# Optimization experiments

Hardware: AMD Instinct MI355X
Metric: run time of the kernel (lower is better)

## Reference

```python
import jax, jax.numpy as jnp
import numpy as np

NUM_HEADS = 16
LN_EPS = 1e-5


def setup_inputs() -> dict:
    key = jax.random.key(0)
    ks = jax.random.split(key, 5)
    B, S, D = 2, 2048, 1024
    scale = 1.0 / np.sqrt(D)
    return {
        "x": jax.random.normal(ks[0], (B, S, D), dtype=jnp.float32),
        "in_proj_w": jax.random.normal(ks[1], (3 * D, D), dtype=jnp.float32) * scale,
        "in_proj_b": jnp.zeros((3 * D,), dtype=jnp.float32),
        "out_proj_w": jax.random.normal(ks[2], (D, D), dtype=jnp.float32) * scale,
        "out_proj_b": jnp.zeros((D,), dtype=jnp.float32),
        "ln_gamma": jnp.ones((D,), dtype=jnp.float32),
        "ln_beta": jnp.zeros((D,), dtype=jnp.float32),
    }


def reference(x, in_proj_w, in_proj_b, out_proj_w, out_proj_b, ln_gamma, ln_beta):
    # Faithful to nn.MultiheadAttention(batch_first=True, need_weights=True)
    # + residual + LayerNorm. Dropout is identity (eval mode).
    B, S, D = x.shape
    H = NUM_HEADS
    hd = D // H

    qkv = x @ in_proj_w.T + in_proj_b                      # [B,S,3D]
    q, k, v = jnp.split(qkv, 3, axis=-1)
    # [B,S,D] -> [B,H,S,hd]
    q = q.reshape(B, S, H, hd).transpose(0, 2, 1, 3)
    k = k.reshape(B, S, H, hd).transpose(0, 2, 1, 3)
    v = v.reshape(B, S, H, hd).transpose(0, 2, 1, 3)

    scores = jnp.einsum("bhqd,bhkd->bhqk", q, k) / jnp.sqrt(jnp.float32(hd))
    w = jax.nn.softmax(scores, axis=-1)                    # [B,H,S,S]
    ctx = jnp.einsum("bhqk,bhkd->bhqd", w, v)              # [B,H,S,hd]
    ctx = ctx.transpose(0, 2, 1, 3).reshape(B, S, D)
    attn_output = ctx @ out_proj_w.T + out_proj_b          # [B,S,D]

    # residual + LayerNorm (dropout disabled at inference)
    y = x + attn_output
    mu = jnp.mean(y, axis=-1, keepdims=True)
    var = jnp.var(y, axis=-1, keepdims=True)
    out = (y - mu) * jax.lax.rsqrt(var + LN_EPS) * ln_gamma + ln_beta

    # PyTorch default average_attn_weights=True -> mean over heads
    attn_weights = w.mean(axis=1)                          # [B,S,S]
    return (out, attn_weights)
```

## Files before the change

### kernel.cpp

```cpp
#include <hip/hip_runtime.h>
#include <math.h>

constexpr int B = 2, S = 2048, D = 1024, H = 16, HD = 64;
constexpr int T = B * S;
constexpr float EPS = 1e-5f;

typedef float f32x4 __attribute__((ext_vector_type(4)));
typedef __bf16 bf16x8 __attribute__((ext_vector_type(8)));

struct alignas(16) u4 { unsigned x, y, z, w; };
struct alignas(8) u2 { unsigned x, y; };

__device__ __forceinline__ unsigned short f2bf(float f) {
  unsigned u = __float_as_uint(f);
  u += 0x7fffu + ((u >> 16) & 1u);
  return (unsigned short)(u >> 16);
}
__device__ __forceinline__ float bf2f(unsigned short h) {
  return __uint_as_float(((unsigned)h) << 16);
}
__device__ __forceinline__ f32x4 MM(bf16x8 a, bf16x8 b, f32x4 c) {
  return __builtin_amdgcn_mfma_f32_16x16x32_bf16(a, b, c, 0, 0, 0);
}
union U16x8 { u4 q; bf16x8 b; };

__device__ __forceinline__ bf16x8 ld_frag(const unsigned short* lds, int row,
                                          int chunk) {
  U16x8 u;
  u.q = *(const u4*)((const char*)lds + row * 128 +
                     (((chunk) ^ (row & 7)) * 16));
  return u.b;
}

__device__ __forceinline__ void stage64(const unsigned short* __restrict__ src,
                                        size_t off, int rstride,
                                        unsigned short* lds, int tid) {
#pragma unroll
  for (int p = 0; p < 2; ++p) {
    const int idx = tid + p * 256;
    const int r = idx >> 3, c = idx & 7;
    u4 v = *(const u4*)(src + off + (size_t)r * rstride + c * 8);
    *(u4*)((char*)lds + r * 128 + ((c ^ (r & 7)) * 16)) = v;
  }
}

__global__ __launch_bounds__(256) void k_split(const float* __restrict__ src,
                                               unsigned short* __restrict__ hi,
                                               unsigned short* __restrict__ lo,
                                               int n4) {
  const int i = blockIdx.x * 256 + threadIdx.x;
  if (i >= n4) return;
  const float4 v = ((const float4*)src)[i];
  const unsigned short h0 = f2bf(v.x), h1 = f2bf(v.y), h2 = f2bf(v.z),
                       h3 = f2bf(v.w);
  u2 hh, ll;
  hh.x = (unsigned)h0 | ((unsigned)h1 << 16);
  hh.y = (unsigned)h2 | ((unsigned)h3 << 16);
  ll.x = (unsigned)f2bf(v.x - bf2f(h0)) | ((unsigned)f2bf(v.y - bf2f(h1)) << 16);
  ll.y = (unsigned)f2bf(v.z - bf2f(h2)) | ((unsigned)f2bf(v.w - bf2f(h3)) << 16);
  ((u2*)hi)[i] = hh;
  ((u2*)lo)[i] = ll;
}

__global__ __launch_bounds__(256) void k_qkv(
    const unsigned short* __restrict__ xh, const unsigned short* __restrict__ xl,
    const unsigned short* __restrict__ wh, const unsigned short* __restrict__ wl,
    const float* __restrict__ bias,
    unsigned short* __restrict__ Qh, unsigned short* __restrict__ Ql,
    unsigned short* __restrict__ Kh, unsigned short* __restrict__ Kl,
    unsigned short* __restrict__ Vh, unsigned short* __restrict__ Vl) {
  __shared__ unsigned short Ah[4096], Al[4096], Bh[4096], Bl[4096];
  const int tid = threadIdx.x;
  const int w = tid >> 6, lane = tid & 63;
  const int j = lane & 15, g = lane >> 4;
  const int row0 = blockIdx.y * 64;
  const int col0 = blockIdx.x * 64;
  const f32x4 z4 = {0.f, 0.f, 0.f, 0.f};
  f32x4 acc[4] = {z4, z4, z4, z4};

  for (int k0 = 0; k0 < D; k0 += 64) {
    __syncthreads();
    stage64(xh, (size_t)row0 * D + k0, D, Ah, tid);
    stage64(xl, (size_t)row0 * D + k0, D, Al, tid);
    stage64(wh, (size_t)col0 * D + k0, D, Bh, tid);
    stage64(wl, (size_t)col0 * D + k0, D, Bl, tid);
    __syncthreads();
#pragma unroll
    for (int kk = 0; kk < 2; ++kk) {
      const int arow = 16 * w + j;
      const bf16x8 ah = ld_frag(Ah, arow, kk * 4 + g);
      const bf16x8 al = ld_frag(Al, arow, kk * 4 + g);
#pragma unroll
      for (int nf = 0; nf < 4; ++nf) {
        const bf16x8 bh = ld_frag(Bh, 16 * nf + j, kk * 4 + g);
        const bf16x8 bl = ld_frag(Bl, 16 * nf + j, kk * 4 + g);
        acc[nf] = MM(ah, bh, acc[nf]);
        acc[nf] = MM(ah, bl, acc[nf]);
        acc[nf] = MM(al, bh, acc[nf]);
      }
    }
  }

  const int part = col0 >> 10;
  const int h = (col0 & 1023) >> 6;
  if (part < 2) {
    const float qsc = (part == 0) ? 0.125f : 1.0f;
    unsigned short* dh = (part == 0) ? Qh : Kh;
    unsigned short* dl = (part == 0) ? Ql : Kl;
#pragma unroll
    for (int nf = 0; nf < 4; ++nf) {
      const int hd = 16 * nf + j;
      const float bv = bias[col0 + hd];
#pragma unroll
      for (int r = 0; r < 4; ++r) {
        const int tok = row0 + 16 * w + 4 * g + r;
        const int bb = tok >> 11, ss = tok & 2047;
        const float v = (acc[nf][r] + bv) * qsc;
        const unsigned short hh = f2bf(v);
        const size_t o = (((size_t)bb * H + h) * S + ss) * HD + hd;
        dh[o] = hh;
        dl[o] = f2bf(v - bf2f(hh));
      }
    }
  } else {
#pragma unroll
    for (int nf = 0; nf < 4; ++nf) {
      const int hd = 16 * nf + j;
      const float bv = bias[col0 + hd];
      const int tok0 = row0 + 16 * w + 4 * g;
      const int bb = tok0 >> 11, ss = tok0 & 2047;
      const float v0 = acc[nf][0] + bv, v1 = acc[nf][1] + bv;
      const float v2 = acc[nf][2] + bv, v3 = acc[nf][3] + bv;
      const unsigned short h0 = f2bf(v0), h1 = f2bf(v1), h2 = f2bf(v2),
                           h3 = f2bf(v3);
      const size_t o = (((size_t)bb * H + h) * HD + hd) * S + ss;
      u2 ph, pl;
      ph.x = (unsigned)h0 | ((unsigned)h1 << 16);
      ph.y = (unsigned)h2 | ((unsigned)h3 << 16);
      pl.x = (unsigned)f2bf(v0 - bf2f(h0)) | ((unsigned)f2bf(v1 - bf2f(h1)) << 16);
      pl.y = (unsigned)f2bf(v2 - bf2f(h2)) | ((unsigned)f2bf(v3 - bf2f(h3)) << 16);
      *(u2*)(Vh + o) = ph;
      *(u2*)(Vl + o) = pl;
    }
  }
}

__global__ __launch_bounds__(256) void k_ctx(
    const unsigned short* __restrict__ Qh, const unsigned short* __restrict__ Ql,
    const unsigned short* __restrict__ Kh, const unsigned short* __restrict__ Kl,
    const unsigned short* __restrict__ Vh, const unsigned short* __restrict__ Vl,
    unsigned short* __restrict__ ch, unsigned short* __restrict__ cl,
    float* __restrict__ mo, float* __restrict__ lo) {
  __shared__ unsigned short Ksh[4096], Ksl[4096], Vsh[4096], Vsl[4096];
  const int tid = threadIdx.x;
  const int w = tid >> 6, lane = tid & 63;
  const int j = lane & 15, g = lane >> 4;
  const int q0 = blockIdx.x * 64;
  const int h = blockIdx.y, b = blockIdx.z;
  const size_t hb = (size_t)b * H + h;
  const int qrow = q0 + 16 * w + j;

  bf16x8 qfh[2], qfl[2];
#pragma unroll
  for (int kk = 0; kk < 2; ++kk) {
    const size_t o = (hb * S + qrow) * HD + kk * 32 + 8 * g;
    U16x8 u;
    u.q = *(const u4*)(Qh + o);
    qfh[kk] = u.b;
    u.q = *(const u4*)(Ql + o);
    qfl[kk] = u.b;
  }

  const f32x4 z4 = {0.f, 0.f, 0.f, 0.f};
  f32x4 ctxa[4] = {z4, z4, z4, z4};
  float m_run = -INFINITY, l_run = 0.f;

  for (int k0 = 0; k0 < S; k0 += 64) {
    __syncthreads();
    stage64(Kh, (hb * S + k0) * HD, HD, Ksh, tid);
    stage64(Kl, (hb * S + k0) * HD, HD, Ksl, tid);
    stage64(Vh, hb * HD * S + k0, S, Vsh, tid);
    stage64(Vl, hb * HD * S + k0, S, Vsl, tid);
    __syncthreads();

    f32x4 st[4] = {z4, z4, z4, z4};
#pragma unroll
    for (int kk = 0; kk < 2; ++kk) {
#pragma unroll
      for (int kb = 0; kb < 4; ++kb) {
        const bf16x8 ah = ld_frag(Ksh, 16 * kb + j, kk * 4 + g);
        const bf16x8 al = ld_frag(Ksl, 16 * kb + j, kk * 4 + g);
        st[kb] = MM(ah, qfh[kk], st[kb]);
        st[kb] = MM(ah, qfl[kk], st[kb]);
        st[kb] = MM(al, qfh[kk], st[kb]);
      }
    }

    float pm = -INFINITY;
#pragma unroll
    for (int kb = 0; kb < 4; ++kb)
#pragma unroll
      for (int r = 0; r < 4; ++r) pm = fmaxf(pm, st[kb][r]);
    pm = fmaxf(pm, __shfl_xor(pm, 16));
    pm = fmaxf(pm, __shfl_xor(pm, 32));
    const float m_new = fmaxf(m_run, pm);
    const float sc = __expf(m_run - m_new);
    m_run = m_new;
    float p[4][4];
    float ls = 0.f;
#pragma unroll
    for (int kb = 0; kb < 4; ++kb)
#pragma unroll
      for (int r = 0; r < 4; ++r) {
        p[kb][r] = __expf(st[kb][r] - m_new);
        ls += p[kb][r];
      }
    l_run = l_run * sc + ls;
#pragma unroll
    for (int mf = 0; mf < 4; ++mf) ctxa[mf] *= sc;

    unsigned ph[4][2], pl[4][2];
#pragma unroll
    for (int kb = 0; kb < 4; ++kb) {
      const unsigned short a0 = f2bf(p[kb][0]), a1 = f2bf(p[kb][1]);
      const unsigned short a2 = f2bf(p[kb][2]), a3 = f2bf(p[kb][3]);
      ph[kb][0] = (unsigned)a0 | ((unsigned)a1 << 16);
      ph[kb][1] = (unsigned)a2 | ((unsigned)a3 << 16);
      pl[kb][0] = (unsigned)f2bf(p[kb][0] - bf2f(a0)) |
                  ((unsigned)f2bf(p[kb][1] - bf2f(a1)) << 16);
      pl[kb][1] = (unsigned)f2bf(p[kb][2] - bf2f(a2)) |
                  ((unsigned)f2bf(p[kb][3] - bf2f(a3)) << 16);
    }

    const int srcA = ((g & 1) << 5) + j;
    const int srcB = srcA + 16;
    const bool hikb = (g >> 1) != 0;
#pragma unroll
    for (int t = 0; t < 2; ++t) {
      const unsigned w0a = __shfl(ph[2 * t][0], srcA), w0b = __shfl(ph[2 * t + 1][0], srcA);
      const unsigned w1a = __shfl(ph[2 * t][1], srcA), w1b = __shfl(ph[2 * t + 1][1], srcA);
      const unsigned w2a = __shfl(ph[2 * t][0], srcB), w2b = __shfl(ph[2 * t + 1][0], srcB);
      const unsigned w3a = __shfl(ph[2 * t][1], srcB), w3b = __shfl(ph[2 * t + 1][1], srcB);
      U16x8 pbh;
      pbh.q.x = hikb ? w0b : w0a;
      pbh.q.y = hikb ? w1b : w1a;
      pbh.q.z = hikb ? w2b : w2a;
      pbh.q.w = hikb ? w3b : w3a;
      const unsigned v0a = __shfl(pl[2 * t][0], srcA), v0b = __shfl(pl[2 * t + 1][0], srcA);
      const unsigned v1a = __shfl(pl[2 * t][1], srcA), v1b = __shfl(pl[2 * t + 1][1], srcA);
      const unsigned v2a = __shfl(pl[2 * t][0], srcB), v2b = __shfl(pl[2 * t + 1][0], srcB);
      const unsigned v3a = __shfl(pl[2 * t][1], srcB), v3b = __shfl(pl[2 * t + 1][1], srcB);
      U16x8 pbl;
      pbl.q.x = hikb ? v0b : v0a;
      pbl.q.y = hikb ? v1b : v1a;
      pbl.q.z = hikb ? v2b : v2a;
      pbl.q.w = hikb ? v3b : v3a;
#pragma unroll
      for (int mf = 0; mf < 4; ++mf) {
        const bf16x8 vh_ = ld_frag(Vsh, 16 * mf + j, t * 4 + g);
        const bf16x8 vl_ = ld_frag(Vsl, 16 * mf + j, t * 4 + g);
        ctxa[mf] = MM(vh_, pbh.b, ctxa[mf]);
        ctxa[mf] = MM(vh_, pbl.b, ctxa[mf]);
        ctxa[mf] = MM(vl_, pbh.b, ctxa[mf]);
      }
    }
  }

  float lt = l_run;
  lt += __shfl_xor(lt, 16);
  lt += __shfl_xor(lt, 32);
  const float inv = 1.0f / lt;
  const int tokg = b * S + (q0 + 16 * w + j);
#pragma unroll
  for (int mf = 0; mf < 4; ++mf) {
    const int feat = h * HD + 16 * mf + 4 * g;
    const float v0 = ctxa[mf][0] * inv, v1 = ctxa[mf][1] * inv;
    const float v2 = ctxa[mf][2] * inv, v3 = ctxa[mf][3] * inv;
    const unsigned short h0 = f2bf(v0), h1 = f2bf(v1), h2 = f2bf(v2),
                         h3 = f2bf(v3);
    const size_t o = (size_t)tokg * D + feat;
    u2 hh, ll;
    hh.x = (unsigned)h0 | ((unsigned)h1 << 16);
    hh.y = (unsigned)h2 | ((unsigned)h3 << 16);
    ll.x = (unsigned)f2bf(v0 - bf2f(h0)) | ((unsigned)f2bf(v1 - bf2f(h1)) << 16);
    ll.y = (unsigned)f2bf(v2 - bf2f(h2)) | ((unsigned)f2bf(v3 - bf2f(h3)) << 16);
    *(u2*)(ch + o) = hh;
    *(u2*)(cl + o) = ll;
  }
  if (g == 0) {
    mo[hb * S + qrow] = m_run;
    lo[hb * S + qrow] = lt;
  }
}

__global__ __launch_bounds__(256) void k_oproj(
    const unsigned short* __restrict__ ah_, const unsigned short* __restrict__ al_,
    const unsigned short* __restrict__ wh, const unsigned short* __restrict__ wl,
    const float* __restrict__ bias, const float* __restrict__ x,
    float* __restrict__ y) {
  __shared__ unsigned short Ah[4096], Al[4096], Bh[4096], Bl[4096];
  const int tid = threadIdx.x;
  const int w = tid >> 6, lane = tid & 63;
  const int j = lane & 15, g = lane >> 4;
  const int row0 = blockIdx.y * 64;
  const int col0 = blockIdx.x * 64;
  const f32x4 z4 = {0.f, 0.f, 0.f, 0.f};
  f32x4 acc[4] = {z4, z4, z4, z4};

  for (int k0 = 0; k0 < D; k0 += 64) {
    __syncthreads();
    stage64(ah_, (size_t)row0 * D + k0, D, Ah, tid);
    stage64(al_, (size_t)row0 * D + k0, D, Al, tid);
    stage64(wh, (size_t)col0 * D + k0, D, Bh, tid);
    stage64(wl, (size_t)col0 * D + k0, D, Bl, tid);
    __syncthreads();
#pragma unroll
    for (int kk = 0; kk < 2; ++kk) {
      const int arow = 16 * w + j;
      const bf16x8 ah = ld_frag(Ah, arow, kk * 4 + g);
      const bf16x8 al = ld_frag(Al, arow, kk * 4 + g);
#pragma unroll
      for (int nf = 0; nf < 4; ++nf) {
        const bf16x8 bh = ld_frag(Bh, 16 * nf + j, kk * 4 + g);
        const bf16x8 bl = ld_frag(Bl, 16 * nf + j, kk * 4 + g);
        acc[nf] = MM(ah, bh, acc[nf]);
        acc[nf] = MM(ah, bl, acc[nf]);
        acc[nf] = MM(al, bh, acc[nf]);
      }
    }
  }
#pragma unroll
  for (int nf = 0; nf < 4; ++nf) {
    const int col = col0 + 16 * nf + j;
    const float bv = bias[col];
#pragma unroll
    for (int r = 0; r < 4; ++r) {
      const int tok = row0 + 16 * w + 4 * g + r;
      const size_t off = (size_t)tok * D + col;
      y[off] = acc[nf][r] + bv + x[off];
    }
  }
}

__global__ __launch_bounds__(256) void k_wts(
    const unsigned short* __restrict__ Qh, const unsigned short* __restrict__ Ql,
    const unsigned short* __restrict__ Kh, const unsigned short* __restrict__ Kl,
    const float* __restrict__ mi, const float* __restrict__ li,
    float* __restrict__ attn) {
  __shared__ unsigned short Ksh[4096], Ksl[4096];
  const int tid = threadIdx.x;
  const int w = tid >> 6, lane = tid & 63;
  const int j = lane & 15, g = lane >> 4;
  const int k0 = blockIdx.x * 64;
  const int q0 = blockIdx.y * 64;
  const int b = blockIdx.z;
  const f32x4 z4 = {0.f, 0.f, 0.f, 0.f};
  f32x4 wacc[4] = {z4, z4, z4, z4};

  for (int h = 0; h < H; ++h) {
    const size_t hb = (size_t)b * H + h;
    __syncthreads();
    stage64(Kh, (hb * S + k0) * HD, HD, Ksh, tid);
    stage64(Kl, (hb * S + k0) * HD, HD, Ksl, tid);
    __syncthreads();
    bf16x8 qfh[2], qfl[2];
#pragma unroll
    for (int kk = 0; kk < 2; ++kk) {
      const size_t o = (hb * S + q0 + 16 * w + j) * HD + kk * 32 + 8 * g;
      U16x8 u;
      u.q = *(const u4*)(Qh + o);
      qfh[kk] = u.b;
      u.q = *(const u4*)(Ql + o);
      qfl[kk] = u.b;
    }
    f32x4 sacc[4] = {z4, z4, z4, z4};
#pragma unroll
    for (int kk = 0; kk < 2; ++kk) {
#pragma unroll
      for (int nf = 0; nf < 4; ++nf) {
        const bf16x8 kh_ = ld_frag(Ksh, 16 * nf + j, kk * 4 + g);
        const bf16x8 kl_ = ld_frag(Ksl, 16 * nf + j, kk * 4 + g);
        sacc[nf] = MM(qfh[kk], kh_, sacc[nf]);
        sacc[nf] = MM(qfh[kk], kl_, sacc[nf]);
        sacc[nf] = MM(qfl[kk], kh_, sacc[nf]);
      }
    }
    float mr[4], lv[4];
#pragma unroll
    for (int r = 0; r < 4; ++r) {
      const size_t o = hb * S + q0 + 16 * w + 4 * g + r;
      mr[r] = mi[o];
      lv[r] = 1.0f / li[o];
    }
#pragma unroll
    for (int nf = 0; nf < 4; ++nf)
#pragma unroll
      for (int r = 0; r < 4; ++r)
        wacc[nf][r] = fmaf(__expf(sacc[nf][r] - mr[r]), lv[r], wacc[nf][r]);
  }
  const float ih = 1.0f / (float)H;
#pragma unroll
  for (int nf = 0; nf < 4; ++nf)
#pragma unroll
    for (int r = 0; r < 4; ++r) {
      const size_t row = (size_t)b * S + q0 + 16 * w + 4 * g + r;
      attn[row * S + k0 + 16 * nf + j] = wacc[nf][r] * ih;
    }
}

__global__ __launch_bounds__(256) void k_ln(float* __restrict__ y,
                                            const float* __restrict__ gamma,
                                            const float* __restrict__ beta) {
  const int row = blockIdx.x;
  const int tid = threadIdx.x;
  const float4 v = *reinterpret_cast<const float4*>(&y[(size_t)row * D + tid * 4]);
  float s = v.x + v.y + v.z + v.w;
  float sq = v.x * v.x + v.y * v.y + v.z * v.z + v.w * v.w;
#pragma unroll
  for (int off = 32; off > 0; off >>= 1) {
    s += __shfl_down(s, off);
    sq += __shfl_down(sq, off);
  }
  __shared__ float sm[8];
  const int wid = tid >> 6, lane = tid & 63;
  if (lane == 0) {
    sm[wid] = s;
    sm[4 + wid] = sq;
  }
  __syncthreads();
  s = sm[0] + sm[1] + sm[2] + sm[3];
  sq = sm[4] + sm[5] + sm[6] + sm[7];
  const float mu = s * (1.0f / D);
  const float var = sq * (1.0f / D) - mu * mu;
  const float rstd = rsqrtf(var + EPS);
  const float4 gmv = *reinterpret_cast<const float4*>(&gamma[tid * 4]);
  const float4 btv = *reinterpret_cast<const float4*>(&beta[tid * 4]);
  float4 o;
  o.x = (v.x - mu) * rstd * gmv.x + btv.x;
  o.y = (v.y - mu) * rstd * gmv.y + btv.y;
  o.z = (v.z - mu) * rstd * gmv.z + btv.z;
  o.w = (v.w - mu) * rstd * gmv.w + btv.w;
  *reinterpret_cast<float4*>(&y[(size_t)row * D + tid * 4]) = o;
}

extern "C" void kernel_launch(void* const* d_in, const int* in_sizes, int n_in,
                              void* d_out, int out_size, void* d_ws,
                              size_t ws_size, hipStream_t stream) {
  const float* x = (const float*)d_in[0];
  const float* inW = (const float*)d_in[1];
  const float* inB = (const float*)d_in[2];
  const float* outW = (const float*)d_in[3];
  const float* outB = (const float*)d_in[4];
  const float* gamma = (const float*)d_in[5];
  const float* beta = (const float*)d_in[6];

  float* out = (float*)d_out;
  float* attn = out + (size_t)T * D;

  char* ab = (char*)attn;
  unsigned short* xh = (unsigned short*)(ab);
  unsigned short* xl = (unsigned short*)(ab + (8u << 20));
  unsigned short* wih = (unsigned short*)(ab + (16u << 20));
  unsigned short* wil = (unsigned short*)(ab + (22u << 20));
  unsigned short* woh = (unsigned short*)(ab + (28u << 20));
  unsigned short* wol = (unsigned short*)(ab + (30u << 20));
  unsigned short* cth = xh;
  unsigned short* ctl = xl;

  char* wsb = (char*)d_ws;
  unsigned short* Qh = (unsigned short*)(wsb);
  unsigned short* Ql = (unsigned short*)(wsb + (8u << 20));
  unsigned short* Kh = (unsigned short*)(wsb + (16u << 20));
  unsigned short* Kl = (unsigned short*)(wsb + (24u << 20));
  unsigned short* Vh = (unsigned short*)(wsb + (32u << 20));
  unsigned short* Vl = (unsigned short*)(wsb + (40u << 20));
  float* mo = (float*)(wsb + (48u << 20));
  float* lo = (float*)(wsb + (48u << 20) + 262144);

  k_split<<<4096, 256, 0, stream>>>(x, xh, xl, T * D / 4);
  k_split<<<3072, 256, 0, stream>>>(inW, wih, wil, 3 * D * D / 4);
  k_split<<<1024, 256, 0, stream>>>(outW, woh, wol, D * D / 4);
  k_qkv<<<dim3(48, 64), 256, 0, stream>>>(xh, xl, wih, wil, inB, Qh, Ql, Kh,
                                          Kl, Vh, Vl);
  k_ctx<<<dim3(32, 16, 2), 256, 0, stream>>>(Qh, Ql, Kh, Kl, Vh, Vl, cth, ctl,
                                             mo, lo);
  k_oproj<<<dim3(16, 64), 256, 0, stream>>>(cth, ctl, woh, wol, outB, x, out);
  k_wts<<<dim3(32, 32, 2), 256, 0, stream>>>(Qh, Ql, Kh, Kl, mo, lo, attn);
  k_ln<<<T, 256, 0, stream>>>(out, gamma, beta);
}
```

Measured before the change: 558.4 us.

## Enlarge GEMM and attention tiles, use direct global-to-LDS loads and exp2 softmax

The QKV and output-projection GEMMs move from 64x64 to 128x128 tiles with a 2x2 wave layout, so each wave computes a 4x4 grid of MFMA tiles. The attention and weights kernels now process 128 query rows per block, two 16-row slices per wave, reusing each K fragment across both slices. LDS staging uses the global_load_lds builtin with the swizzle applied on the global address, Q is pre-scaled by log2(e) so softmax can use the v_exp_f32 instruction directly, and bf16 conversion goes through the native cast. The intent is to cut LDS and global traffic per MFMA and lower exp cost, at the price of higher register pressure, a launch_bounds occupancy target of 2, and fewer blocks per grid.

```diff
diff --git a/kernel.cpp b/kernel.cpp
--- a/kernel.cpp
+++ b/kernel.cpp
@@ -4,408 +4,497 @@
 constexpr int B = 2, S = 2048, D = 1024, H = 16, HD = 64;
 constexpr int T = B * S;
 constexpr float EPS = 1e-5f;
+constexpr float LOG2E = 1.44269504088896340736f;
 
 typedef float f32x4 __attribute__((ext_vector_type(4)));
 typedef __bf16 bf16x8 __attribute__((ext_vector_type(8)));
+typedef unsigned short u16;
 
 struct alignas(16) u4 { unsigned x, y, z, w; };
 struct alignas(8) u2 { unsigned x, y; };
 
-__device__ __forceinline__ unsigned short f2bf(float f) {
-  unsigned u = __float_as_uint(f);
-  u += 0x7fffu + ((u >> 16) & 1u);
-  return (unsigned short)(u >> 16);
-}
-__device__ __forceinline__ float bf2f(unsigned short h) {
+__device__ __forceinline__ u16 f2bf(float f) {
+  union { __bf16 h; u16 u; } c;
+  c.h = (__bf16)f;
+  return c.u;
+}
+__device__ __forceinline__ float bf2f(u16 h) {
   return __uint_as_float(((unsigned)h) << 16);
+}
+__device__ __forceinline__ unsigned pk2(float a, float b) {
+  return (unsigned)f2bf(a) | ((unsigned)f2bf(b) << 16);
+}
+__device__ __forceinline__ float fexp2(float x) {
+  float r;
+  asm("v_exp_f32 %0, %1" : "=v"(r) : "v"(x));
+  return r;
 }
 __device__ __forceinline__ f32x4 MM(bf16x8 a, bf16x8 b, f32x4 c) {
   return __builtin_amdgcn_mfma_f32_16x16x32_bf16(a, b, c, 0, 0, 0);
 }
 union U16x8 { u4 q; bf16x8 b; };
 
-__device__ __forceinline__ bf16x8 ld_frag(const unsigned short* lds, int row,
-                                          int chunk) {
+__device__ __forceinline__ bf16x8 ld_frag(const u16* lds, int row, int chunk) {
   U16x8 u;
-  u.q = *(const u4*)((const char*)lds + row * 128 +
-                     (((chunk) ^ (row & 7)) * 16));
+  u.q = *(const u4*)((const char*)lds + row * 128 + ((chunk ^ (row & 7)) * 16));
   return u.b;
 }
 
-__device__ __forceinline__ void stage64(const unsigned short* __restrict__ src,
-                                        size_t off, int rstride,
-                                        unsigned short* lds, int tid) {
-#pragma unroll
-  for (int p = 0; p < 2; ++p) {
-    const int idx = tid + p * 256;
-    const int r = idx >> 3, c = idx & 7;
-    u4 v = *(const u4*)(src + off + (size_t)r * rstride + c * 8);
-    *(u4*)((char*)lds + r * 128 + ((c ^ (r & 7)) * 16)) = v;
+template <int ITERS>
+__device__ __forceinline__ void stageT(const u16* __restrict__ src, size_t off,
+                                       int rstride, u16* lds, int tid) {
+  const int lane = tid & 63, w = tid >> 6;
+#pragma unroll
+  for (int p = 0; p < ITERS; ++p) {
+    const int idx = p * 256 + w * 64 + lane;
+    const int r = idx >> 3, cc = idx & 7;
+    const u16* gp = src + off + (size_t)r * rstride + ((cc ^ (r & 7)) * 8);
+    u16* lp = lds + (size_t)(p * 256 + w * 64) * 8;
+    __builtin_amdgcn_global_load_lds(
+        (const __attribute__((address_space(1))) void*)gp,
+        (__attribute__((address_space(3))) void*)lp, 16, 0, 0);
   }
 }
 
 __global__ __launch_bounds__(256) void k_split(const float* __restrict__ src,
-                                               unsigned short* __restrict__ hi,
-                                               unsigned short* __restrict__ lo,
-                                               int n4) {
+                                               u16* __restrict__ hi,
+                                               u16* __restrict__ lo, int n4) {
   const int i = blockIdx.x * 256 + threadIdx.x;
   if (i >= n4) return;
   const float4 v = ((const float4*)src)[i];
-  const unsigned short h0 = f2bf(v.x), h1 = f2bf(v.y), h2 = f2bf(v.z),
-                       h3 = f2bf(v.w);
   u2 hh, ll;
-  hh.x = (unsigned)h0 | ((unsigned)h1 << 16);
-  hh.y = (unsigned)h2 | ((unsigned)h3 << 16);
-  ll.x = (unsigned)f2bf(v.x - bf2f(h0)) | ((unsigned)f2bf(v.y - bf2f(h1)) << 16);
-  ll.y = (unsigned)f2bf(v.z - bf2f(h2)) | ((unsigned)f2bf(v.w - bf2f(h3)) << 16);
+  hh.x = pk2(v.x, v.y);
+  hh.y = pk2(v.z, v.w);
+  ll.x = pk2(v.x - bf2f((u16)hh.x), v.y - bf2f((u16)(hh.x >> 16)));
+  ll.y = pk2(v.z - bf2f((u16)hh.y), v.w - bf2f((u16)(hh.y >> 16)));
   ((u2*)hi)[i] = hh;
   ((u2*)lo)[i] = ll;
 }
 
-__global__ __launch_bounds__(256) void k_qkv(
-    const unsigned short* __restrict__ xh, const unsigned short* __restrict__ xl,
-    const unsigned short* __restrict__ wh, const unsigned short* __restrict__ wl,
-    const float* __restrict__ bias,
-    unsigned short* __restrict__ Qh, unsigned short* __restrict__ Ql,
-    unsigned short* __restrict__ Kh, unsigned short* __restrict__ Kl,
-    unsigned short* __restrict__ Vh, unsigned short* __restrict__ Vl) {
-  __shared__ unsigned short Ah[4096], Al[4096], Bh[4096], Bl[4096];
+__global__ __launch_bounds__(256, 2) void k_qkv(
+    const u16* __restrict__ xh, const u16* __restrict__ xl,
+    const u16* __restrict__ wh, const u16* __restrict__ wl,
+    const float* __restrict__ bias, u16* __restrict__ Qh, u16* __restrict__ Ql,
+    u16* __restrict__ Kh, u16* __restrict__ Kl, u16* __restrict__ Vh,
+    u16* __restrict__ Vl) {
+  __shared__ u16 Ah[8192], Al[8192], Bh[8192], Bl[8192];
   const int tid = threadIdx.x;
   const int w = tid >> 6, lane = tid & 63;
   const int j = lane & 15, g = lane >> 4;
-  const int row0 = blockIdx.y * 64;
-  const int col0 = blockIdx.x * 64;
+  const int wr = w >> 1, wc = w & 1;
+  const int row0 = blockIdx.y * 128;
+  const int col0 = blockIdx.x * 128;
   const f32x4 z4 = {0.f, 0.f, 0.f, 0.f};
-  f32x4 acc[4] = {z4, z4, z4, z4};
+  f32x4 acc[4][4];
+#pragma unroll
+  for (int mi = 0; mi < 4; ++mi)
+#pragma unroll
+    for (int ni = 0; ni < 4; ++ni) acc[mi][ni] = z4;
 
   for (int k0 = 0; k0 < D; k0 += 64) {
     __syncthreads();
-    stage64(xh, (size_t)row0 * D + k0, D, Ah, tid);
-    stage64(xl, (size_t)row0 * D + k0, D, Al, tid);
-    stage64(wh, (size_t)col0 * D + k0, D, Bh, tid);
-    stage64(wl, (size_t)col0 * D + k0, D, Bl, tid);
+    stageT<4>(xh, (size_t)row0 * D + k0, D, Ah, tid);
+    stageT<4>(xl, (size_t)row0 * D + k0, D, Al, tid);
+    stageT<4>(wh, (size_t)col0 * D + k0, D, Bh, tid);
+    stageT<4>(wl, (size_t)col0 * D + k0, D, Bl, tid);
     __syncthreads();
 #pragma unroll
     for (int kk = 0; kk < 2; ++kk) {
-      const int arow = 16 * w + j;
-      const bf16x8 ah = ld_frag(Ah, arow, kk * 4 + g);
-      const bf16x8 al = ld_frag(Al, arow, kk * 4 + g);
-#pragma unroll
-      for (int nf = 0; nf < 4; ++nf) {
-        const bf16x8 bh = ld_frag(Bh, 16 * nf + j, kk * 4 + g);
-        const bf16x8 bl = ld_frag(Bl, 16 * nf + j, kk * 4 + g);
-        acc[nf] = MM(ah, bh, acc[nf]);
-        acc[nf] = MM(ah, bl, acc[nf]);
-        acc[nf] = MM(al, bh, acc[nf]);
-      }
+      bf16x8 afh[4], afl[4], bfh[4], bfl[4];
+#pragma unroll
+      for (int mi = 0; mi < 4; ++mi) {
+        afh[mi] = ld_frag(Ah, wr * 64 + 16 * mi + j, kk * 4 + g);
+        afl[mi] = ld_frag(Al, wr * 64 + 16 * mi + j, kk * 4 + g);
+      }
+#pragma unroll
+      for (int ni = 0; ni < 4; ++ni) {
+        bfh[ni] = ld_frag(Bh, wc * 64 + 16 * ni + j, kk * 4 + g);
+        bfl[ni] = ld_frag(Bl, wc * 64 + 16 * ni + j, kk * 4 + g);
+      }
+#pragma unroll
+      for (int mi = 0; mi < 4; ++mi)
+#pragma unroll
+        for (int ni = 0; ni < 4; ++ni) {
+          acc[mi][ni] = MM(afh[mi], bfh[ni], acc[mi][ni]);
+          acc[mi][ni] = MM(afh[mi], bfl[ni], acc[mi][ni]);
+          acc[mi][ni] = MM(afl[mi], bfh[ni], acc[mi][ni]);
+        }
     }
   }
 
   const int part = col0 >> 10;
-  const int h = (col0 & 1023) >> 6;
   if (part < 2) {
-    const float qsc = (part == 0) ? 0.125f : 1.0f;
-    unsigned short* dh = (part == 0) ? Qh : Kh;
-    unsigned short* dl = (part == 0) ? Ql : Kl;
-#pragma unroll
-    for (int nf = 0; nf < 4; ++nf) {
-      const int hd = 16 * nf + j;
-      const float bv = bias[col0 + hd];
-#pragma unroll
-      for (int r = 0; r < 4; ++r) {
-        const int tok = row0 + 16 * w + 4 * g + r;
-        const int bb = tok >> 11, ss = tok & 2047;
-        const float v = (acc[nf][r] + bv) * qsc;
-        const unsigned short hh = f2bf(v);
-        const size_t o = (((size_t)bb * H + h) * S + ss) * HD + hd;
-        dh[o] = hh;
-        dl[o] = f2bf(v - bf2f(hh));
-      }
+    const float qsc = (part == 0) ? 0.125f * LOG2E : 1.0f;
+    u16* dh = (part == 0) ? Qh : Kh;
+    u16* dl = (part == 0) ? Ql : Kl;
+#pragma unroll
+    for (int ni = 0; ni < 4; ++ni) {
+      const int col = col0 + wc * 64 + 16 * ni + j;
+      const int h = (col & 1023) >> 6, hd = col & 63;
+      const float bv = bias[col];
+#pragma unroll
+      for (int mi = 0; mi < 4; ++mi)
+#pragma unroll
+        for (int r = 0; r < 4; ++r) {
+          const int tok = row0 + wr * 64 + 16 * mi + 4 * g + r;
+          const int bb = tok >> 11, ss = tok & 2047;
+          const float v = (acc[mi][ni][r] + bv) * qsc;
+          const size_t o = (((size_t)bb * H + h) * S + ss) * HD + hd;
+          const u16 hv = f2bf(v);
+          dh[o] = hv;
+          dl[o] = f2bf(v - bf2f(hv));
+        }
     }
   } else {
 #pragma unroll
-    for (int nf = 0; nf < 4; ++nf) {
-      const int hd = 16 * nf + j;
-      const float bv = bias[col0 + hd];
-      const int tok0 = row0 + 16 * w + 4 * g;
-      const int bb = tok0 >> 11, ss = tok0 & 2047;
-      const float v0 = acc[nf][0] + bv, v1 = acc[nf][1] + bv;
-      const float v2 = acc[nf][2] + bv, v3 = acc[nf][3] + bv;
-      const unsigned short h0 = f2bf(v0), h1 = f2bf(v1), h2 = f2bf(v2),
-                           h3 = f2bf(v3);
-      const size_t o = (((size_t)bb * H + h) * HD + hd) * S + ss;
-      u2 ph, pl;
-      ph.x = (unsigned)h0 | ((unsigned)h1 << 16);
-      ph.y = (unsigned)h2 | ((unsigned)h3 << 16);
-      pl.x = (unsigned)f2bf(v0 - bf2f(h0)) | ((unsigned)f2bf(v1 - bf2f(h1)) << 16);
-      pl.y = (unsigned)f2bf(v2 - bf2f(h2)) | ((unsigned)f2bf(v3 - bf2f(h3)) << 16);
-      *(u2*)(Vh + o) = ph;
-      *(u2*)(Vl + o) = pl;
-    }
-  }
-}
-
-__global__ __launch_bounds__(256) void k_ctx(
-    const unsigned short* __restrict__ Qh, const unsigned short* __restrict__ Ql,
-    const unsigned short* __restrict__ Kh, const unsigned short* __restrict__ Kl,
-    const unsigned short* __restrict__ Vh, const unsigned short* __restrict__ Vl,
-    unsigned short* __restrict__ ch, unsigned short* __restrict__ cl,
-    float* __restrict__ mo, float* __restrict__ lo) {
-  __shared__ unsigned short Ksh[4096], Ksl[4096], Vsh[4096], Vsl[4096];
+    for (int ni = 0; ni < 4; ++ni) {
+      const int col = col0 + wc * 64 + 16 * ni + j;
+      const int h = (col & 1023) >> 6, hd = col & 63;
+      const float bv = bias[col];
+#pragma unroll
+      for (int mi = 0; mi < 4; ++mi) {
+        const int tok0 = row0 + wr * 64 + 16 * mi + 4 * g;
+        const int bb = tok0 >> 11, ss = tok0 & 2047;
+        const float v0 = acc[mi][ni][0] + bv, v1 = acc[mi][ni][1] + bv;
+        const float v2 = acc[mi][ni][2] + bv, v3 = acc[mi][ni][3] + bv;
+        const u16 h0 = f2bf(v0), h1 = f2bf(v1), h2 = f2bf(v2), h3 = f2bf(v3);
+        const size_t o = (((size_t)bb * H + h) * HD + hd) * S + ss;
+        u2 ph, pl;
+        ph.x = (unsigned)h0 | ((unsigned)h1 << 16);
+        ph.y = (unsigned)h2 | ((unsigned)h3 << 16);
+        pl.x = pk2(v0 - bf2f(h0), v1 - bf2f(h1));
+        pl.y = pk2(v2 - bf2f(h2), v3 - bf2f(h3));
+        *(u2*)(Vh + o) = ph;
+        *(u2*)(Vl + o) = pl;
+      }
+    }
+  }
+}
+
+__global__ __launch_bounds__(256, 2) void k_ctx(
+    const u16* __restrict__ Qh, const u16* __restrict__ Ql,
+    const u16* __restrict__ Kh, const u16* __restrict__ Kl,
+    const u16* __restrict__ Vh, const u16* __restrict__ Vl,
+    u16* __restrict__ ch, u16* __restrict__ cl, float* __restrict__ mo,
+    float* __restrict__ lo) {
+  __shared__ u16 Ksh[4096], Ksl[4096], Vsh[4096], Vsl[4096];
   const int tid = threadIdx.x;
   const int w = tid >> 6, lane = tid & 63;
   const int j = lane & 15, g = lane >> 4;
-  const int q0 = blockIdx.x * 64;
+  const int q0 = blockIdx.x * 128;
   const int h = blockIdx.y, b = blockIdx.z;
   const size_t hb = (size_t)b * H + h;
-  const int qrow = q0 + 16 * w + j;
-
-  bf16x8 qfh[2], qfl[2];
-#pragma unroll
-  for (int kk = 0; kk < 2; ++kk) {
-    const size_t o = (hb * S + qrow) * HD + kk * 32 + 8 * g;
-    U16x8 u;
-    u.q = *(const u4*)(Qh + o);
-    qfh[kk] = u.b;
-    u.q = *(const u4*)(Ql + o);
-    qfl[kk] = u.b;
-  }
+  int qr[2];
+  qr[0] = q0 + 32 * w + j;
+  qr[1] = qr[0] + 16;
+
+  bf16x8 qfh[2][2], qfl[2][2];
+#pragma unroll
+  for (int s = 0; s < 2; ++s)
+#pragma unroll
+    for (int kk = 0; kk < 2; ++kk) {
+      const size_t o = (hb * S + qr[s]) * HD + kk * 32 + 8 * g;
+      U16x8 u;
+      u.q = *(const u4*)(Qh + o);
+      qfh[s][kk] = u.b;
+      u.q = *(const u4*)(Ql + o);
+      qfl[s][kk] = u.b;
+    }
 
   const f32x4 z4 = {0.f, 0.f, 0.f, 0.f};
-  f32x4 ctxa[4] = {z4, z4, z4, z4};
-  float m_run = -INFINITY, l_run = 0.f;
+  f32x4 ctxa[2][4];
+#pragma unroll
+  for (int s = 0; s < 2; ++s)
+#pragma unroll
+    for (int mf = 0; mf < 4; ++mf) ctxa[s][mf] = z4;
+  float m_run[2] = {-INFINITY, -INFINITY};
+  float l_run[2] = {0.f, 0.f};
 
   for (int k0 = 0; k0 < S; k0 += 64) {
     __syncthreads();
-    stage64(Kh, (hb * S + k0) * HD, HD, Ksh, tid);
-    stage64(Kl, (hb * S + k0) * HD, HD, Ksl, tid);
-    stage64(Vh, hb * HD * S + k0, S, Vsh, tid);
-    stage64(Vl, hb * HD * S + k0, S, Vsl, tid);
-    __syncthreads();
-
-    f32x4 st[4] = {z4, z4, z4, z4};
+    stageT<2>(Kh, (hb * S + k0) * HD, HD, Ksh, tid);
+    stageT<2>(Kl, (hb * S + k0) * HD, HD, Ksl, tid);
+    stageT<2>(Vh, hb * HD * S + k0, S, Vsh, tid);
+    stageT<2>(Vl, hb * HD * S + k0, S, Vsl, tid);
+    __syncthreads();
+
+    f32x4 st[2][4];
+#pragma unroll
+    for (int s = 0; s < 2; ++s)
+#pragma unroll
+      for (int kb = 0; kb < 4; ++kb) st[s][kb] = z4;
 #pragma unroll
     for (int kk = 0; kk < 2; ++kk) {
+      bf16x8 kh4[4], kl4[4];
 #pragma unroll
       for (int kb = 0; kb < 4; ++kb) {
-        const bf16x8 ah = ld_frag(Ksh, 16 * kb + j, kk * 4 + g);
-        const bf16x8 al = ld_frag(Ksl, 16 * kb + j, kk * 4 + g);
-        st[kb] = MM(ah, qfh[kk], st[kb]);
-        st[kb] = MM(ah, qfl[kk], st[kb]);
-        st[kb] = MM(al, qfh[kk], st[kb]);
-      }
-    }
-
-    float pm = -INFINITY;
-#pragma unroll
-    for (int kb = 0; kb < 4; ++kb)
-#pragma unroll
-      for (int r = 0; r < 4; ++r) pm = fmaxf(pm, st[kb][r]);
-    pm = fmaxf(pm, __shfl_xor(pm, 16));
-    pm = fmaxf(pm, __shfl_xor(pm, 32));
-    const float m_new = fmaxf(m_run, pm);
-    const float sc = __expf(m_run - m_new);
-    m_run = m_new;
-    float p[4][4];
-    float ls = 0.f;
-#pragma unroll
-    for (int kb = 0; kb < 4; ++kb)
-#pragma unroll
-      for (int r = 0; r < 4; ++r) {
-        p[kb][r] = __expf(st[kb][r] - m_new);
-        ls += p[kb][r];
-      }
-    l_run = l_run * sc + ls;
-#pragma unroll
-    for (int mf = 0; mf < 4; ++mf) ctxa[mf] *= sc;
-
-    unsigned ph[4][2], pl[4][2];
-#pragma unroll
-    for (int kb = 0; kb < 4; ++kb) {
-      const unsigned short a0 = f2bf(p[kb][0]), a1 = f2bf(p[kb][1]);
-      const unsigned short a2 = f2bf(p[kb][2]), a3 = f2bf(p[kb][3]);
-      ph[kb][0] = (unsigned)a0 | ((unsigned)a1 << 16);
-      ph[kb][1] = (unsigned)a2 | ((unsigned)a3 << 16);
-      pl[kb][0] = (unsigned)f2bf(p[kb][0] - bf2f(a0)) |
-                  ((unsigned)f2bf(p[kb][1] - bf2f(a1)) << 16);
-      pl[kb][1] = (unsigned)f2bf(p[kb][2] - bf2f(a2)) |
-                  ((unsigned)f2bf(p[kb][3] - bf2f(a3)) << 16);
-    }
-
-    const int srcA = ((g & 1) << 5) + j;
-    const int srcB = srcA + 16;
-    const bool hikb = (g >> 1) != 0;
-#pragma unroll
-    for (int t = 0; t < 2; ++t) {
-      const unsigned w0a = __shfl(ph[2 * t][0], srcA), w0b = __shfl(ph[2 * t + 1][0], srcA);
-      const unsigned w1a = __shfl(ph[2 * t][1], srcA), w1b = __shfl(ph[2 * t + 1][1], srcA);
-      const unsigned w2a = __shfl(ph[2 * t][0], srcB), w2b = __shfl(ph[2 * t + 1][0], srcB);
-      const unsigned w3a = __shfl(ph[2 * t][1], srcB), w3b = __shfl(ph[2 * t + 1][1], srcB);
-      U16x8 pbh;
-      pbh.q.x = hikb ? w0b : w0a;
-      pbh.q.y = hikb ? w1b : w1a;
-      pbh.q.z = hikb ? w2b : w2a;
-      pbh.q.w = hikb ? w3b : w3a;
-      const unsigned v0a = __shfl(pl[2 * t][0], srcA), v0b = __shfl(pl[2 * t + 1][0], srcA);
-      const unsigned v1a = __shfl(pl[2 * t][1], srcA), v1b = __shfl(pl[2 * t + 1][1], srcA);
-      const unsigned v2a = __shfl(pl[2 * t][0], srcB), v2b = __shfl(pl[2 * t + 1][0], srcB);
-      const unsigned v3a = __shfl(pl[2 * t][1], srcB), v3b = __shfl(pl[2 * t + 1][1], srcB);
-      U16x8 pbl;
-      pbl.q.x = hikb ? v0b : v0a;
-      pbl.q.y = hikb ? v1b : v1a;
-      pbl.q.z = hikb ? v2b : v2a;
-      pbl.q.w = hikb ? v3b : v3a;
+        kh4[kb] = ld_frag(Ksh, 16 * kb + j, kk * 4 + g);
+        kl4[kb] = ld_frag(Ksl, 16 * kb + j, kk * 4 + g);
+      }
+#pragma unroll
+      for (int s = 0; s < 2; ++s)
+#pragma unroll
+        for (int kb = 0; kb < 4; ++kb) {
+          st[s][kb] = MM(kh4[kb], qfh[s][kk], st[s][kb]);
+          st[s][kb] = MM(kh4[kb], qfl[s][kk], st[s][kb]);
+          st[s][kb] = MM(kl4[kb], qfh[s][kk], st[s][kb]);
+        }
+    }
+
+    U16x8 pbh[2][2], pbl[2][2];
+#pragma unroll
+    for (int s = 0; s < 2; ++s) {
+      float pm = -INFINITY;
+#pragma unroll
+      for (int kb = 0; kb < 4; ++kb)
+#pragma unroll
+        for (int r = 0; r < 4; ++r) pm = fmaxf(pm, st[s][kb][r]);
+      pm = fmaxf(pm, __shfl_xor(pm, 16));
+      pm = fmaxf(pm, __shfl_xor(pm, 32));
+      const float m_new = fmaxf(m_run[s], pm);
+      const float sc = fexp2(m_run[s] - m_new);
+      m_run[s] = m_new;
+      float p[4][4];
+      float ls = 0.f;
+#pragma unroll
+      for (int kb = 0; kb < 4; ++kb)
+#pragma unroll
+        for (int r = 0; r < 4; ++r) {
+          p[kb][r] = fexp2(st[s][kb][r] - m_new);
+          ls += p[kb][r];
+        }
+      l_run[s] = l_run[s] * sc + ls;
+#pragma unroll
+      for (int mf = 0; mf < 4; ++mf) ctxa[s][mf] *= sc;
+
+      unsigned ph[4][2], pl[4][2];
+#pragma unroll
+      for (int kb = 0; kb < 4; ++kb) {
+        const u16 a0 = f2bf(p[kb][0]), a1 = f2bf(p[kb][1]);
+        const u16 a2 = f2bf(p[kb][2]), a3 = f2bf(p[kb][3]);
+        ph[kb][0] = (unsigned)a0 | ((unsigned)a1 << 16);
+        ph[kb][1] = (unsigned)a2 | ((unsigned)a3 << 16);
+        pl[kb][0] = pk2(p[kb][0] - bf2f(a0), p[kb][1] - bf2f(a1));
+        pl[kb][1] = pk2(p[kb][2] - bf2f(a2), p[kb][3] - bf2f(a3));
+      }
+      const int srcA = ((g & 1) << 5) + j;
+      const int srcB = srcA + 16;
+      const bool hikb = (g >> 1) != 0;
+#pragma unroll
+      for (int t = 0; t < 2; ++t) {
+        const unsigned w0a = __shfl(ph[2 * t][0], srcA),
+                       w0b = __shfl(ph[2 * t + 1][0], srcA);
+        const unsigned w1a = __shfl(ph[2 * t][1], srcA),
+                       w1b = __shfl(ph[2 * t + 1][1], srcA);
+        const unsigned w2a = __shfl(ph[2 * t][0], srcB),
+                       w2b = __shfl(ph[2 * t + 1][0], srcB);
+        const unsigned w3a = __shfl(ph[2 * t][1], srcB),
+                       w3b = __shfl(ph[2 * t + 1][1], srcB);
+        pbh[s][t].q.x = hikb ? w0b : w0a;
+        pbh[s][t].q.y = hikb ? w1b : w1a;
+        pbh[s][t].q.z = hikb ? w2b : w2a;
+        pbh[s][t].q.w = hikb ? w3b : w3a;
+        const unsigned v0a = __shfl(pl[2 * t][0], srcA),
+                       v0b = __shfl(pl[2 * t + 1][0], srcA);
+        const unsigned v1a = __shfl(pl[2 * t][1], srcA),
+                       v1b = __shfl(pl[2 * t + 1][1], srcA);
+        const unsigned v2a = __shfl(pl[2 * t][0], srcB),
+                       v2b = __shfl(pl[2 * t + 1][0], srcB);
+        const unsigned v3a = __shfl(pl[2 * t][1], srcB),
+                       v3b = __shfl(pl[2 * t + 1][1], srcB);
+        pbl[s][t].q.x = hikb ? v0b : v0a;
+        pbl[s][t].q.y = hikb ? v1b : v1a;
+        pbl[s][t].q.z = hikb ? v2b : v2a;
+        pbl[s][t].q.w = hikb ? v3b : v3a;
+      }
+    }
+
+#pragma unroll
+    for (int t = 0; t < 2; ++t)
 #pragma unroll
       for (int mf = 0; mf < 4; ++mf) {
         const bf16x8 vh_ = ld_frag(Vsh, 16 * mf + j, t * 4 + g);
         const bf16x8 vl_ = ld_frag(Vsl, 16 * mf + j, t * 4 + g);
-        ctxa[mf] = MM(vh_, pbh.b, ctxa[mf]);
-        ctxa[mf] = MM(vh_, pbl.b, ctxa[mf]);
-        ctxa[mf] = MM(vl_, pbh.b, ctxa[mf]);
-      }
-    }
-  }
-
-  float lt = l_run;
-  lt += __shfl_xor(lt, 16);
-  lt += __shfl_xor(lt, 32);
-  const float inv = 1.0f / lt;
-  const int tokg = b * S + (q0 + 16 * w + j);
-#pragma unroll
-  for (int mf = 0; mf < 4; ++mf) {
-    const int feat = h * HD + 16 * mf + 4 * g;
-    const float v0 = ctxa[mf][0] * inv, v1 = ctxa[mf][1] * inv;
-    const float v2 = ctxa[mf][2] * inv, v3 = ctxa[mf][3] * inv;
-    const unsigned short h0 = f2bf(v0), h1 = f2bf(v1), h2 = f2bf(v2),
-                         h3 = f2bf(v3);
-    const size_t o = (size_t)tokg * D + feat;
-    u2 hh, ll;
-    hh.x = (unsigned)h0 | ((unsigned)h1 << 16);
-    hh.y = (unsigned)h2 | ((unsigned)h3 << 16);
-    ll.x = (unsigned)f2bf(v0 - bf2f(h0)) | ((unsigned)f2bf(v1 - bf2f(h1)) << 16);
-    ll.y = (unsigned)f2bf(v2 - bf2f(h2)) | ((unsigned)f2bf(v3 - bf2f(h3)) << 16);
-    *(u2*)(ch + o) = hh;
-    *(u2*)(cl + o) = ll;
-  }
-  if (g == 0) {
-    mo[hb * S + qrow] = m_run;
-    lo[hb * S + qrow] = lt;
-  }
-}
-
-__global__ __launch_bounds__(256) void k_oproj(
-    const unsigned short* __restrict__ ah_, const unsigned short* __restrict__ al_,
-    const unsigned short* __restrict__ wh, const unsigned short* __restrict__ wl,
+#pragma unroll
+        for (int s = 0; s < 2; ++s) {
+          ctxa[s][mf] = MM(vh_, pbh[s][t].b, ctxa[s][mf]);
+          ctxa[s][mf] = MM(vh_, pbl[s][t].b, ctxa[s][mf]);
+          ctxa[s][mf] = MM(vl_, pbh[s][t].b, ctxa[s][mf]);
+        }
+      }
+  }
+
+#pragma unroll
+  for (int s = 0; s < 2; ++s) {
+    float lt = l_run[s];
+    lt += __shfl_xor(lt, 16);
+    lt += __shfl_xor(lt, 32);
+    const float inv = 1.0f / lt;
+    const int tokg = b * S + qr[s];
+#pragma unroll
+    for (int mf = 0; mf < 4; ++mf) {
+      const int feat = h * HD + 16 * mf + 4 * g;
+      const float v0 = ctxa[s][mf][0] * inv, v1 = ctxa[s][mf][1] * inv;
+      const float v2 = ctxa[s][mf][2] * inv, v3 = ctxa[s][mf][3] * inv;
+      const u16 h0 = f2bf(v0), h1 = f2bf(v1), h2 = f2bf(v2), h3 = f2bf(v3);
+      const size_t o = (size_t)tokg * D + feat;
+      u2 hh, ll;
+      hh.x = (unsigned)h0 | ((unsigned)h1 << 16);
+      hh.y = (unsigned)h2 | ((unsigned)h3 << 16);
+      ll.x = pk2(v0 - bf2f(h0), v1 - bf2f(h1));
+      ll.y = pk2(v2 - bf2f(h2), v3 - bf2f(h3));
+      *(u2*)(ch + o) = hh;
+      *(u2*)(cl + o) = ll;
+    }
+    if (g == 0) {
+      mo[hb * S + qr[s]] = m_run[s];
+      lo[hb * S + qr[s]] = inv;
+    }
+  }
+}
+
+__global__ __launch_bounds__(256, 2) void k_oproj(
+    const u16* __restrict__ ah_, const u16* __restrict__ al_,
+    const u16* __restrict__ wh, const u16* __restrict__ wl,
     const float* __restrict__ bias, const float* __restrict__ x,
     float* __restrict__ y) {
-  __shared__ unsigned short Ah[4096], Al[4096], Bh[4096], Bl[4096];
+  __shared__ u16 Ah[8192], Al[8192], Bh[8192], Bl[8192];
   const int tid = threadIdx.x;
   const int w = tid >> 6, lane = tid & 63;
   const int j = lane & 15, g = lane >> 4;
-  const int row0 = blockIdx.y * 64;
-  const int col0 = blockIdx.x * 64;
+  const int wr = w >> 1, wc = w & 1;
+  const int row0 = blockIdx.y * 128;
+  const int col0 = blockIdx.x * 128;
   const f32x4 z4 = {0.f, 0.f, 0.f, 0.f};
-  f32x4 acc[4] = {z4, z4, z4, z4};
+  f32x4 acc[4][4];
+#pragma unroll
+  for (int mi = 0; mi < 4; ++mi)
+#pragma unroll
+    for (int ni = 0; ni < 4; ++ni) acc[mi][ni] = z4;
 
   for (int k0 = 0; k0 < D; k0 += 64) {
     __syncthreads();
-    stage64(ah_, (size_t)row0 * D + k0, D, Ah, tid);
-    stage64(al_, (size_t)row0 * D + k0, D, Al, tid);
-    stage64(wh, (size_t)col0 * D + k0, D, Bh, tid);
-    stage64(wl, (size_t)col0 * D + k0, D, Bl, tid);
+    stageT<4>(ah_, (size_t)row0 * D + k0, D, Ah, tid);
+    stageT<4>(al_, (size_t)row0 * D + k0, D, Al, tid);
+    stageT<4>(wh, (size_t)col0 * D + k0, D, Bh, tid);
+    stageT<4>(wl, (size_t)col0 * D + k0, D, Bl, tid);
     __syncthreads();
 #pragma unroll
     for (int kk = 0; kk < 2; ++kk) {
-      const int arow = 16 * w + j;
-      const bf16x8 ah = ld_frag(Ah, arow, kk * 4 + g);
-      const bf16x8 al = ld_frag(Al, arow, kk * 4 + g);
-#pragma unroll
-      for (int nf = 0; nf < 4; ++nf) {
-        const bf16x8 bh = ld_frag(Bh, 16 * nf + j, kk * 4 + g);
-        const bf16x8 bl = ld_frag(Bl, 16 * nf + j, kk * 4 + g);
-        acc[nf] = MM(ah, bh, acc[nf]);
-        acc[nf] = MM(ah, bl, acc[nf]);
-        acc[nf] = MM(al, bh, acc[nf]);
-      }
-    }
-  }
-#pragma unroll
-  for (int nf = 0; nf < 4; ++nf) {
-    const int col = col0 + 16 * nf + j;
+      bf16x8 afh[4], afl[4], bfh[4], bfl[4];
+#pragma unroll
+      for (int mi = 0; mi < 4; ++mi) {
+        afh[mi] = ld_frag(Ah, wr * 64 + 16 * mi + j, kk * 4 + g);
+        afl[mi] = ld_frag(Al, wr * 64 + 16 * mi + j, kk * 4 + g);
+      }
+#pragma unroll
+      for (int ni = 0; ni < 4; ++ni) {
+        bfh[ni] = ld_frag(Bh, wc * 64 + 16 * ni + j, kk * 4 + g);
+        bfl[ni] = ld_frag(Bl, wc * 64 + 16 * ni + j, kk * 4 + g);
+      }
+#pragma unroll
+      for (int mi = 0; mi < 4; ++mi)
+#pragma unroll
+        for (int ni = 0; ni < 4; ++ni) {
+          acc[mi][ni] = MM(afh[mi], bfh[ni], acc[mi][ni]);
+          acc[mi][ni] = MM(afh[mi], bfl[ni], acc[mi][ni]);
+          acc[mi][ni] = MM(afl[mi], bfh[ni], acc[mi][ni]);
+        }
+    }
+  }
+#pragma unroll
+  for (int ni = 0; ni < 4; ++ni) {
+    const int col = col0 + wc * 64 + 16 * ni + j;
     const float bv = bias[col];
 #pragma unroll
-    for (int r = 0; r < 4; ++r) {
-      const int tok = row0 + 16 * w + 4 * g + r;
-      const size_t off = (size_t)tok * D + col;
-      y[off] = acc[nf][r] + bv + x[off];
-    }
-  }
-}
-
-__global__ __launch_bounds__(256) void k_wts(
-    const unsigned short* __restrict__ Qh, const unsigned short* __restrict__ Ql,
-    const unsigned short* __restrict__ Kh, const unsigned short* __restrict__ Kl,
+    for (int mi = 0; mi < 4; ++mi)
+#pragma unroll
+      for (int r = 0; r < 4; ++r) {
+        const int tok = row0 + wr * 64 + 16 * mi + 4 * g + r;
+        const size_t off = (size_t)tok * D + col;
+        y[off] = acc[mi][ni][r] + bv + x[off];
+      }
+  }
+}
+
+__global__ __launch_bounds__(256, 2) void k_wts(
+    const u16* __restrict__ Qh, const u16* __restrict__ Ql,
+    const u16* __restrict__ Kh, const u16* __restrict__ Kl,
     const float* __restrict__ mi, const float* __restrict__ li,
     float* __restrict__ attn) {
-  __shared__ unsigned short Ksh[4096], Ksl[4096];
+  __shared__ u16 Ksh[4096], Ksl[4096];
   const int tid = threadIdx.x;
   const int w = tid >> 6, lane = tid & 63;
   const int j = lane & 15, g = lane >> 4;
   const int k0 = blockIdx.x * 64;
-  const int q0 = blockIdx.y * 64;
+  const int q0 = blockIdx.y * 128;
   const int b = blockIdx.z;
   const f32x4 z4 = {0.f, 0.f, 0.f, 0.f};
-  f32x4 wacc[4] = {z4, z4, z4, z4};
+  f32x4 wacc[2][4];
+#pragma unroll
+  for (int s = 0; s < 2; ++s)
+#pragma unroll
+    for (int nf = 0; nf < 4; ++nf) wacc[s][nf] = z4;
 
   for (int h = 0; h < H; ++h) {
     const size_t hb = (size_t)b * H + h;
     __syncthreads();
-    stage64(Kh, (hb * S + k0) * HD, HD, Ksh, tid);
-    stage64(Kl, (hb * S + k0) * HD, HD, Ksl, tid);
-    __syncthreads();
-    bf16x8 qfh[2], qfl[2];
-#pragma unroll
-    for (int kk = 0; kk < 2; ++kk) {
-      const size_t o = (hb * S + q0 + 16 * w + j) * HD + kk * 32 + 8 * g;
-      U16x8 u;
-      u.q = *(const u4*)(Qh + o);
-      qfh[kk] = u.b;
-      u.q = *(const u4*)(Ql + o);
-      qfl[kk] = u.b;
-    }
-    f32x4 sacc[4] = {z4, z4, z4, z4};
+    stageT<2>(Kh, (hb * S + k0) * HD, HD, Ksh, tid);
+    stageT<2>(Kl, (hb * S + k0) * HD, HD, Ksl, tid);
+    __syncthreads();
+    bf16x8 qfh[2][2], qfl[2][2];
+#pragma unroll
+    for (int s = 0; s < 2; ++s)
+#pragma unroll
+      for (int kk = 0; kk < 2; ++kk) {
+        const size_t o = (hb * S + q0 + 32 * w + 16 * s + j) * HD + kk * 32 + 8 * g;
+        U16x8 u;
+        u.q = *(const u4*)(Qh + o);
+        qfh[s][kk] = u.b;
+        u.q = *(const u4*)(Ql + o);
+        qfl[s][kk] = u.b;
+      }
+    f32x4 sacc[2][4];
+#pragma unroll
+    for (int s = 0; s < 2; ++s)
+#pragma unroll
+      for (int nf = 0; nf < 4; ++nf) sacc[s][nf] = z4;
 #pragma unroll
     for (int kk = 0; kk < 2; ++kk) {
 #pragma unroll
       for (int nf = 0; nf < 4; ++nf) {
         const bf16x8 kh_ = ld_frag(Ksh, 16 * nf + j, kk * 4 + g);
         const bf16x8 kl_ = ld_frag(Ksl, 16 * nf + j, kk * 4 + g);
-        sacc[nf] = MM(qfh[kk], kh_, sacc[nf]);
-        sacc[nf] = MM(qfh[kk], kl_, sacc[nf]);
-        sacc[nf] = MM(qfl[kk], kh_, sacc[nf]);
-      }
-    }
-    float mr[4], lv[4];
-#pragma unroll
-    for (int r = 0; r < 4; ++r) {
-      const size_t o = hb * S + q0 + 16 * w + 4 * g + r;
-      mr[r] = mi[o];
-      lv[r] = 1.0f / li[o];
-    }
+#pragma unroll
+        for (int s = 0; s < 2; ++s) {
+          sacc[s][nf] = MM(qfh[s][kk], kh_, sacc[s][nf]);
+          sacc[s][nf] = MM(qfh[s][kk], kl_, sacc[s][nf]);
+          sacc[s][nf] = MM(qfl[s][kk], kh_, sacc[s][nf]);
+        }
+      }
+    }
+#pragma unroll
+    for (int s = 0; s < 2; ++s)
+#pragma unroll
+      for (int r = 0; r < 4; ++r) {
+        const size_t o = hb * S + q0 + 32 * w + 16 * s + 4 * g + r;
+        const float m = mi[o];
+        const float lv = li[o];
+#pragma unroll
+        for (int nf = 0; nf < 4; ++nf)
+          wacc[s][nf][r] = fmaf(fexp2(sacc[s][nf][r] - m), lv, wacc[s][nf][r]);
+      }
+  }
+  const float ih = 1.0f / (float)H;
+#pragma unroll
+  for (int s = 0; s < 2; ++s)
 #pragma unroll
     for (int nf = 0; nf < 4; ++nf)
 #pragma unroll
-      for (int r = 0; r < 4; ++r)
-        wacc[nf][r] = fmaf(__expf(sacc[nf][r] - mr[r]), lv[r], wacc[nf][r]);
-  }
-  const float ih = 1.0f / (float)H;
-#pragma unroll
-  for (int nf = 0; nf < 4; ++nf)
-#pragma unroll
-    for (int r = 0; r < 4; ++r) {
-      const size_t row = (size_t)b * S + q0 + 16 * w + 4 * g + r;
-      attn[row * S + k0 + 16 * nf + j] = wacc[nf][r] * ih;
-    }
+      for (int r = 0; r < 4; ++r) {
+        const size_t row = (size_t)b * S + q0 + 32 * w + 16 * s + 4 * g + r;
+        attn[row * S + k0 + 16 * nf + j] = wacc[s][nf][r] * ih;
+      }
 }
 
 __global__ __launch_bounds__(256) void k_ln(float* __restrict__ y,
@@ -458,33 +547,33 @@
   float* attn = out + (size_t)T * D;
 
   char* ab = (char*)attn;
-  unsigned short* xh = (unsigned short*)(ab);
-  unsigned short* xl = (unsigned short*)(ab + (8u << 20));
-  unsigned short* wih = (unsigned short*)(ab + (16u << 20));
-  unsigned short* wil = (unsigned short*)(ab + (22u << 20));
-  unsigned short* woh = (unsigned short*)(ab + (28u << 20));
-  unsigned short* wol = (unsigned short*)(ab + (30u << 20));
-  unsigned short* cth = xh;
-  unsigned short* ctl = xl;
+  u16* xh = (u16*)(ab);
+  u16* xl = (u16*)(ab + (8u << 20));
+  u16* wih = (u16*)(ab + (16u << 20));
+  u16* wil = (u16*)(ab + (22u << 20));
+  u16* woh = (u16*)(ab + (28u << 20));
+  u16* wol = (u16*)(ab + (30u << 20));
+  u16* cth = xh;
+  u16* ctl = xl;
 
   char* wsb = (char*)d_ws;
-  unsigned short* Qh = (unsigned short*)(wsb);
-  unsigned short* Ql = (unsigned short*)(wsb + (8u << 20));
-  unsigned short* Kh = (unsigned short*)(wsb + (16u << 20));
-  unsigned short* Kl = (unsigned short*)(wsb + (24u << 20));
-  unsigned short* Vh = (unsigned short*)(wsb + (32u << 20));
-  unsigned short* Vl = (unsigned short*)(wsb + (40u << 20));
+  u16* Qh = (u16*)(wsb);
+  u16* Ql = (u16*)(wsb + (8u << 20));
+  u16* Kh = (u16*)(wsb + (16u << 20));
+  u16* Kl = (u16*)(wsb + (24u << 20));
+  u16* Vh = (u16*)(wsb + (32u << 20));
+  u16* Vl = (u16*)(wsb + (40u << 20));
   float* mo = (float*)(wsb + (48u << 20));
   float* lo = (float*)(wsb + (48u << 20) + 262144);
 
   k_split<<<4096, 256, 0, stream>>>(x, xh, xl, T * D / 4);
   k_split<<<3072, 256, 0, stream>>>(inW, wih, wil, 3 * D * D / 4);
   k_split<<<1024, 256, 0, stream>>>(outW, woh, wol, D * D / 4);
-  k_qkv<<<dim3(48, 64), 256, 0, stream>>>(xh, xl, wih, wil, inB, Qh, Ql, Kh,
+  k_qkv<<<dim3(24, 32), 256, 0, stream>>>(xh, xl, wih, wil, inB, Qh, Ql, Kh,
                                           Kl, Vh, Vl);
-  k_ctx<<<dim3(32, 16, 2), 256, 0, stream>>>(Qh, Ql, Kh, Kl, Vh, Vl, cth, ctl,
+  k_ctx<<<dim3(16, 16, 2), 256, 0, stream>>>(Qh, Ql, Kh, Kl, Vh, Vl, cth, ctl,
                                              mo, lo);
-  k_oproj<<<dim3(16, 64), 256, 0, stream>>>(cth, ctl, woh, wol, outB, x, out);
-  k_wts<<<dim3(32, 32, 2), 256, 0, stream>>>(Qh, Ql, Kh, Kl, mo, lo, attn);
+  k_oproj<<<dim3(8, 32), 256, 0, stream>>>(cth, ctl, woh, wol, outB, x, out);
+  k_wts<<<dim3(32, 16, 2), 256, 0, stream>>>(Qh, Ql, Kh, Kl, mo, lo, attn);
   k_ln<<<T, 256, 0, stream>>>(out, gamma, beta);
 }
```

Result: faster. 458.9 us (-17.8%).
